# Performance work log

Hardware: AMD Instinct MI355X
Metric: run time of the kernel (lower is better)

Reference implementation:

```python
import jax, jax.numpy as jnp
from jax import lax
import numpy as np

NUM_ITER = 20
STOP_THRESH = 1e-4
NEG_SLOPE = 0.01


def _min_pool(x, window):
    # min over window == -max_pool(-x); stride 1, SAME padding matches pad=(k-1)//2
    return lax.reduce_window(x, jnp.inf, lax.min, (1, 1) + window, (1,) * 5, 'SAME')


def _max_pool(x, window):
    return lax.reduce_window(x, -jnp.inf, lax.max, (1, 1) + window, (1,) * 5, 'SAME')


def soft_erode(img):
    # kernels: (3,3,3) and (3,3,1) from anisotropy (1,1,0.5); both preserve shape
    e1 = _min_pool(img, (3, 3, 3))
    e2 = _min_pool(img, (3, 3, 1))
    return jnp.minimum(e1, e2)


def soft_dilate(img):
    return _max_pool(img, (3, 3, 3))


def soft_open(img):
    return soft_dilate(soft_erode(img))


def soft_skel(img):
    skel = jax.nn.leaky_relu(img - soft_open(img), NEG_SLOPE)
    prev = jnp.zeros_like(skel)
    active = jnp.asarray(True)

    def step(carry, _):
        cimg, cskel, cprev, cact = carry
        img2 = soft_erode(cimg)
        delta = jax.nn.leaky_relu(img2 - soft_open(img2), NEG_SLOPE)
        upd = jax.nn.leaky_relu(delta - cskel * delta, NEG_SLOPE)
        skel2 = cskel + upd
        dn = jnp.mean(jnp.abs(skel2 - cprev))
        # torch applies the update, THEN checks delta_norm and breaks; so the
        # update is applied whenever we were active entering the iteration.
        img_n = jnp.where(cact, img2, cimg)
        skel_n = jnp.where(cact, skel2, cskel)
        prev_n = jnp.where(cact, skel2, cprev)
        act_n = cact & (dn >= STOP_THRESH)
        return (img_n, skel_n, prev_n, act_n), None

    (_, skel, _, _), _ = lax.scan(step, (img, skel, prev, active), None, length=NUM_ITER)
    return skel


def setup_inputs() -> dict:
    key = jax.random.key(0)
    img = jax.random.uniform(key, (2, 1, 128, 256, 256), dtype=jnp.float32)
    return {"img": img}


def reference(img):
    # distance_transform returns zeros -> sigmoid(0)=0.5 path is absent since the
    # attribute is never set in __init__; forward is just soft_skel.
    return soft_skel(img)
```

## Files before the change

### kernel.cpp

```cpp
#include <hip/hip_runtime.h>
#include <math.h>

#define D_DIM 128
#define H_DIM 256
#define W_DIM 256
#define HW (H_DIM * W_DIM)
#define HW4 (HW / 4)
#define NIMG 2
#define NPI (D_DIM * HW)
#define NTOT (NIMG * NPI)

#define TDZ 32
#define TH 16
#define TW 64

#define AW4R 18
#define AW4 19
#define AH 20
#define EW4R 17
#define EW4 19
#define EH 18

#define NLOADLIN (AH * AW4)
#define NLOADP 384
#define NEPAIR ((EH / 2) * EW4R)

#define NUM_ITER 20
#define STOP_THRESH 1e-4

__device__ __forceinline__ float min3f(float a, float b, float c) { return fminf(fminf(a, b), c); }
__device__ __forceinline__ float max3f(float a, float b, float c) { return fmaxf(fmaxf(a, b), c); }
__device__ __forceinline__ float leaky(float x) { return fmaxf(x, 0.01f * x); }

__device__ __forceinline__ float dpp_shl1(float v) {
    int i = __float_as_int(v);
    int r = __builtin_amdgcn_update_dpp(i, i, 0x101, 0xF, 0xF, false);
    return __int_as_float(r);
}

#define BAR_FULL() do { asm volatile("s_waitcnt vmcnt(0) lgkmcnt(0)" ::: "memory"); \
                        __builtin_amdgcn_s_barrier(); \
                        __builtin_amdgcn_sched_barrier(0); } while (0)
#define BAR_VM4()  do { asm volatile("s_waitcnt vmcnt(4) lgkmcnt(0)" ::: "memory"); \
                        __builtin_amdgcn_s_barrier(); \
                        __builtin_amdgcn_sched_barrier(0); } while (0)
#define BAR_VM2()  do { asm volatile("s_waitcnt vmcnt(2) lgkmcnt(0)" ::: "memory"); \
                        __builtin_amdgcn_s_barrier(); \
                        __builtin_amdgcn_sched_barrier(0); } while (0)
#define BAR_LDS() do { asm volatile("s_waitcnt lgkmcnt(0)" ::: "memory"); \
                       __builtin_amdgcn_s_barrier(); \
                       __builtin_amdgcn_sched_barrier(0); } while (0)

#define GLOAD_LDS(gp, lp) \
    __builtin_amdgcn_global_load_lds((const __attribute__((address_space(1))) unsigned int*)(gp), \
                                     (__attribute__((address_space(3))) unsigned int*)(lp), 16, 0, 0)

__global__ void init_slots(double* slots) {
    int t = threadIdx.x;
    if (t < 32) slots[t] = 0.0;
    if (t >= 32 && t < 36) ((float*)(slots + 32))[t - 32] = INFINITY;
}

__global__ __launch_bounds__(256) void skel_step(
    const float* __restrict__ a_in,
    float* __restrict__ a_out,
    float* __restrict__ skel,
    double* __restrict__ slots,
    int step)
{
    __shared__ float4 aS4[4][NLOADP];
    __shared__ float4 eT4[2][EH * EW4];
    __shared__ float wsum[4];

    const int t = threadIdx.x;

    {
        int act = 1;
        for (int j = 1; j < step; ++j)
            if (!(slots[j] >= STOP_THRESH * (double)NTOT)) { act = 0; break; }
        if (!act) return;
    }

    const float* infp = (const float*)(slots + 32);

    const int lid = blockIdx.x + 4 * (blockIdx.y + 16 * blockIdx.z);
    const int swz = (lid & 7) * 64 + (lid >> 3);
    const int bx = swz & 3;
    const int by = (swz >> 2) & 15;
    const int zz = swz >> 6;
    const int bz = zz & 3, img = zz >> 2;
    const int x0 = bx * TW, y0 = by * TH, z0 = bz * TDZ;

    const float* in = a_in + (size_t)img * NPI;
    float4* aout4 = (float4*)(a_out + (size_t)img * NPI);
    float4* sk4 = (float4*)(skel + (size_t)img * NPI);

    int lOff0; bool lVal0;
    {
        int lr = t / AW4, lc = t - lr * AW4;
        int gy = y0 - 2 + lr, gx = x0 - 4 + 4 * lc;
        lVal0 = (lc < AW4R) && ((unsigned)gy < H_DIM) && ((unsigned)gx <= (unsigned)(W_DIM - 4));
        lOff0 = gy * W_DIM + gx;
    }
    const bool hasL1 = t < 128;
    int lOff1 = 0; bool lVal1 = false;
    if (hasL1) {
        int q = t + 256;
        int lr = q / AW4, lc = q - lr * AW4;
        int gy = y0 - 2 + lr, gx = x0 - 4 + 4 * lc;
        lVal1 = (q < NLOADLIN) && (lc < AW4R) && ((unsigned)gy < H_DIM)
                && ((unsigned)gx <= (unsigned)(W_DIM - 4));
        lOff1 = gy * W_DIM + gx;
    }
    const int wbase = (t >> 6) << 6;

    const bool isE = t < NEPAIR;
    int eRdP = 0, eWrP = 0;
    bool s0A = false, s0B = false, s0C = false, s0D = false;
    bool s1A = false, s1B = false, s1C = false, s1D = false;
    if (isE) {
        int rp = t / EW4R, ej = t - rp * EW4R;
        int mh0 = 2 * rp;
        eRdP = mh0 * AW4 + ej;
        eWrP = mh0 * EW4 + ej;
        int gy0e = y0 - 1 + mh0;
        bool g0 = (unsigned)gy0e < H_DIM;
        bool g1 = (unsigned)(gy0e + 1) < H_DIM;
        int gxb = x0 - 2 + 4 * ej;
        bool xA = (unsigned)(gxb + 0) < W_DIM;
        bool xB = (unsigned)(gxb + 1) < W_DIM;
        bool xC = (unsigned)(gxb + 2) < W_DIM;
        bool xD = (unsigned)(gxb + 3) < W_DIM;
        s0A = g0 && xA; s0B = g0 && xB; s0C = g0 && xC; s0D = g0 && xD;
        s1A = g1 && xA; s1B = g1 && xB; s1C = g1 && xC; s1D = g1 && xD;
    }

    const int oh = t >> 4, wq = t & 15;
    const bool isB = (wq == 15);
    const int oRd = oh * EW4 + wq;
    const int oAc = (oh + 2) * AW4 + wq + 1;
    size_t ob = ((size_t)z0 * HW + (size_t)(y0 + oh) * W_DIM + (size_t)x0) / 4 + wq;

    const float INF = INFINITY;
    const float4 ninf4 = make_float4(-INF, -INF, -INF, -INF);
    const float4 inf4 = make_float4(INF, INF, INF, INF);
    float4 m0P2 = inf4, m0P1 = inf4, m1P2 = inf4, m1P1 = inf4;
    float4 xP2 = ninf4, xP1 = ninf4;
    float4 acP2 = make_float4(0, 0, 0, 0), acP1 = acP2, ecP = acP2;
    float lsum = 0.f;

    for (int s = 0; s < 2; ++s) {
        int z = z0 - 2 + s;
        bool zok = (unsigned)z < D_DIM;
        const float* p = in + (size_t)z * HW;
        const float* s0 = (zok && lVal0) ? (p + lOff0) : infp;
        GLOAD_LDS(s0, &aS4[s][wbase]);
        if (hasL1) {
            const float* s1 = (zok && lVal1) ? (p + lOff1) : infp;
            GLOAD_LDS(s1, &aS4[s][256 + wbase]);
        }
    }

    #define ERODE_SLICE(SLOT, ZPV, DO_E, ETI, P2_0, P1_0, P2_1, P1_1)              \
    do { if (isE) {                                                                \
        const float4* s_ = aS4[SLOT];                                              \
        float4 a0 = s_[eRdP],           b0 = s_[eRdP + 1];                         \
        float4 a1 = s_[eRdP + AW4],     b1 = s_[eRdP + AW4 + 1];                   \
        float4 a2 = s_[eRdP + 2 * AW4], b2 = s_[eRdP + 2 * AW4 + 1];               \
        float4 a3 = s_[eRdP + 3 * AW4], b3 = s_[eRdP + 3 * AW4 + 1];               \
        float4 ma;                                                                 \
        ma.x = fminf(a1.x, a2.x); ma.y = fminf(a1.y, a2.y);                        \
        ma.z = fminf(a1.z, a2.z); ma.w = fminf(a1.w, a2.w);                        \
        float4 v0a, v1a;                                                           \
        v0a.x = fminf(a0.x, ma.x); v0a.y = fminf(a0.y, ma.y);                      \
        v0a.z = fminf(a0.z, ma.z); v0a.w = fminf(a0.w, ma.w);                      \
        v1a.x = fminf(a3.x, ma.x); v1a.y = fminf(a3.y, ma.y);                      \
        v1a.z = fminf(a3.z, ma.z); v1a.w = fminf(a3.w, ma.w);                      \
        float mbx = fminf(b1.x, b2.x), mby = fminf(b1.y, b2.y), mbz = fminf(b1.z, b2.z); \
        float v0bx = fminf(b0.x, mbx), v0by = fminf(b0.y, mby), v0bz = fminf(b0.z, mbz); \
        float v1bx = fminf(b3.x, mbx), v1by = fminf(b3.y, mby), v1bz = fminf(b3.z, mbz); \
        float4 mC0, mC1;                                                           \
        mC0.x = min3f(v0a.y, v0a.z, v0a.w);                                        \
        mC0.y = min3f(v0a.z, v0a.w, v0bx);                                         \
        mC0.z = min3f(v0a.w, v0bx, v0by);                                          \
        mC0.w = min3f(v0bx, v0by, v0bz);                                           \
        mC1.x = min3f(v1a.y, v1a.z, v1a.w);                                        \
        mC1.y = min3f(v1a.z, v1a.w, v1bx);                                         \
        mC1.z = min3f(v1a.w, v1bx, v1by);                                          \
        mC1.w = min3f(v1bx, v1by, v1bz);                                           \
        if ((DO_E) && (ZPV)) {                                                     \
            float4 e;                                                              \
            e.x = s0A ? min3f(P2_0.x, P1_0.x, mC0.x) : -INF;                       \
            e.y = s0B ? min3f(P2_0.y, P1_0.y, mC0.y) : -INF;                       \
            e.z = s0C ? min3f(P2_0.z, P1_0.z, mC0.z) : -INF;                       \
            e.w = s0D ? min3f(P2_0.w, P1_0.w, mC0.w) : -INF;                       \
            eT4[ETI][eWrP] = e;                                                    \
            e.x = s1A ? min3f(P2_1.x, P1_1.x, mC1.x) : -INF;                       \
            e.y = s1B ? min3f(P2_1.y, P1_1.y, mC1.y) : -INF;                       \
            e.z = s1C ? min3f(P2_1.z, P1_1.z, mC1.z) : -INF;                       \
            e.w = s1D ? min3f(P2_1.w, P1_1.w, mC1.w) : -INF;                       \
            eT4[ETI][eWrP + EW4] = e;                                              \
        }                                                                          \
        P2_0 = P1_0; P1_0 = mC0; P2_1 = P1_1; P1_1 = mC1;                          \
    } } while (0)

    #define MAX9(ETI, xCv, ecv)                                                    \
    do {                                                                           \
        const float4* eP_ = eT4[ETI];                                              \
        float4 A0 = eP_[oRd], A1 = eP_[oRd + EW4], A2 = eP_[oRd + 2 * EW4];        \
        float4 B0, B1, B2;                                                         \
        if (isB) {                                                                 \
            B0 = eP_[oRd + 1]; B1 = eP_[oRd + EW4 + 1]; B2 = eP_[oRd + 2 * EW4 + 1]; \
        }                                                                          \
        float4 vm;                                                                 \
        vm.x = max3f(A0.x, A1.x, A2.x); vm.y = max3f(A0.y, A1.y, A2.y);            \
        vm.z = max3f(A0.z, A1.z, A2.z); vm.w = max3f(A0.w, A1.w, A2.w);            \
        float sx = dpp_shl1(vm.x), sy = dpp_shl1(vm.y), sz = dpp_shl1(vm.z);       \
        float c1x = dpp_shl1(A1.x), c1y = dpp_shl1(A1.y);                          \
        float bvx = max3f(B0.x, B1.x, B2.x);                                       \
        float bvy = max3f(B0.y, B1.y, B2.y);                                       \
        float bvz = max3f(B0.z, B1.z, B2.z);                                       \
        float nbx = isB ? bvx : sx;                                                \
        float nby = isB ? bvy : sy;                                                \
        float nbz = isB ? bvz : sz;                                                \
        xCv.x = max3f(vm.y, vm.z, vm.w);                                           \
        xCv.y = max3f(vm.z, vm.w, nbx);                                            \
        xCv.z = max3f(vm.w, nbx, nby);                                             \
        xCv.w = max3f(nbx, nby, nbz);                                              \
        ecv.x = A1.z; ecv.y = A1.w;                                                \
        ecv.z = isB ? B1.x : c1x;                                                  \
        ecv.w = isB ? B1.y : c1y;                                                  \
    } while (0)

    for (int k = 0; k < (TDZ + 4) / 2; ++k) {
        const int i0 = 2 * k, i1 = 2 * k + 1;
        const int slot0 = i0 & 3, slot1 = i1 & 3;

        if (k < 3) { BAR_FULL(); }
        else if (step == NUM_ITER) { BAR_VM2(); }
        else { BAR_VM4(); }

        float4 ggPre0, ggPre1;
        if (step > 0 && i0 >= 4) { ggPre0 = sk4[ob]; ggPre1 = sk4[ob + HW4]; }
        __builtin_amdgcn_sched_barrier(0);

        if (k <= (TDZ + 4) / 2 - 2) {
            for (int s = 0; s < 2; ++s) {
                int z = z0 + 2 * k + s;
                bool zok = (unsigned)z < D_DIM;
                const float* p = in + (size_t)z * HW;
                const float* s0 = (zok && lVal0) ? (p + lOff0) : infp;
                GLOAD_LDS(s0, &aS4[(i0 + 2 + s) & 3][wbase]);
                if (hasL1) {
                    const float* s1 = (zok && lVal1) ? (p + lOff1) : infp;
                    GLOAD_LDS(s1, &aS4[(i0 + 2 + s) & 3][256 + wbase]);
                }
            }
        }
        __builtin_amdgcn_sched_barrier(0);

        const bool zp0 = (unsigned)(z0 - 3 + i0) < D_DIM;
        const bool zp1 = (unsigned)(z0 - 3 + i1) < D_DIM;
        const bool doE = (i0 >= 2);

        ERODE_SLICE(slot0, zp0, doE, 0, m0P2, m0P1, m1P2, m1P1);
        ERODE_SLICE(slot1, zp1, (i1 >= 2), 1, m0P2, m0P1, m1P2, m1P1);

        const float4 aCn0 = aS4[slot0][oAc];
        const float4 aCn1 = aS4[slot1][oAc];

        BAR_LDS();

        {
            float4 xC0, ecB0, xC1, ecB1;
            if (doE && zp0) { MAX9(0, xC0, ecB0); } else { xC0 = ninf4; ecB0 = ninf4; }
            if (doE && zp1) { MAX9(1, xC1, ecB1); } else { xC1 = ninf4; ecB1 = ninf4; }

            if (i0 >= 4) {
                {
                    float4 dl;
                    dl.x = leaky(acP2.x - max3f(xP2.x, xP1.x, xC0.x));
                    dl.y = leaky(acP2.y - max3f(xP2.y, xP1.y, xC0.y));
                    dl.z = leaky(acP2.z - max3f(xP2.z, xP1.z, xC0.z));
                    dl.w = leaky(acP2.w - max3f(xP2.w, xP1.w, xC0.w));
                    if (step < NUM_ITER) aout4[ob] = ecP;
                    if (step == 0) {
                        sk4[ob] = dl;
                    } else {
                        float4 gg = ggPre0, up, gn;
                        up.x = leaky(dl.x - gg.x * dl.x); gn.x = gg.x + up.x;
                        up.y = leaky(dl.y - gg.y * dl.y); gn.y = gg.y + up.y;
                        up.z = leaky(dl.z - gg.z * dl.z); gn.z = gg.z + up.z;
                        up.w = leaky(dl.w - gg.w * dl.w); gn.w = gg.w + up.w;
                        sk4[ob] = gn;
                        if (step == 1)
                            lsum += fabsf(gn.x) + fabsf(gn.y) + fabsf(gn.z) + fabsf(gn.w);
                        else
                            lsum += fabsf(up.x) + fabsf(up.y) + fabsf(up.z) + fabsf(up.w);
                    }
                }
                {
                    float4 dl;
                    dl.x = leaky(acP1.x - max3f(xP1.x, xC0.x, xC1.x));
                    dl.y = leaky(acP1.y - max3f(xP1.y, xC0.y, xC1.y));
                    dl.z = leaky(acP1.z - max3f(xP1.z, xC0.z, xC1.z));
                    dl.w = leaky(acP1.w - max3f(xP1.w, xC0.w, xC1.w));
                    if (step < NUM_ITER) aout4[ob + HW4] = ecB0;
                    if (step == 0) {
                        sk4[ob + HW4] = dl;
                    } else {
                        float4 gg = ggPre1, up, gn;
                        up.x = leaky(dl.x - gg.x * dl.x); gn.x = gg.x + up.x;
                        up.y = leaky(dl.y - gg.y * dl.y); gn.y = gg.y + up.y;
                        up.z = leaky(dl.z - gg.z * dl.z); gn.z = gg.z + up.z;
                        up.w = leaky(dl.w - gg.w * dl.w); gn.w = gg.w + up.w;
                        sk4[ob + HW4] = gn;
                        if (step == 1)
                            lsum += fabsf(gn.x) + fabsf(gn.y) + fabsf(gn.z) + fabsf(gn.w);
                        else
                            lsum += fabsf(up.x) + fabsf(up.y) + fabsf(up.z) + fabsf(up.w);
                    }
                }
                ob += 2 * HW4;
            }
            xP2 = xC0; xP1 = xC1;
            acP2 = aCn0; acP1 = aCn1;
            ecP = ecB1;
        }
    }

    #undef ERODE_SLICE
    #undef MAX9

    if (step > 0) {
        #pragma unroll
        for (int off = 32; off > 0; off >>= 1)
            lsum += __shfl_down(lsum, off, 64);
        const int lane = t & 63, wid = t >> 6;
        if (lane == 0) wsum[wid] = lsum;
        __syncthreads();
        if (t == 0) {
            float b = wsum[0] + wsum[1] + wsum[2] + wsum[3];
            atomicAdd(&slots[step], (double)b);
        }
    }
}

extern "C" void kernel_launch(void* const* d_in, const int* in_sizes, int n_in,
                              void* d_out, int out_size, void* d_ws, size_t ws_size,
                              hipStream_t stream) {
    const float* img = (const float*)d_in[0];
    float* out = (float*)d_out;
    float* buf0 = (float*)d_ws;
    float* buf1 = buf0 + NTOT;
    double* slots = (double*)(buf1 + NTOT);

    init_slots<<<1, 64, 0, stream>>>(slots);

    dim3 grid(W_DIM / TW, H_DIM / TH, (D_DIM / TDZ) * NIMG);
    for (int s = 0; s <= NUM_ITER; ++s) {
        const float* ain = (s == 0) ? img : ((s & 1) ? buf0 : buf1);
        float* aout = (s & 1) ? buf1 : buf0;
        skel_step<<<grid, 256, 0, stream>>>(ain, aout, out, slots, s);
    }
}
```

Measured before the change: 324.8 us.

## Compute two output rows per thread in half-wave layout to share vertical max

The output phase now assigns two adjacent output rows to each active thread, and only the lower 32 lanes of each wave take part. The vertical 3-row max shares the middle two rows between both outputs, cutting LDS reads and max operations per output. The global wait counts grow to match the doubled stores and loads in flight. The trade-off is that half of each wave sits idle in the output stage, and register pressure rises.

```diff
diff --git a/kernel.cpp b/kernel.cpp
--- a/kernel.cpp
+++ b/kernel.cpp
@@ -32,6 +32,13 @@
 __device__ __forceinline__ float max3f(float a, float b, float c) { return fmaxf(fmaxf(a, b), c); }
 __device__ __forceinline__ float leaky(float x) { return fmaxf(x, 0.01f * x); }
 
+__device__ __forceinline__ float4 f4max3v(float4 a, float4 b, float4 c) {
+    float4 r;
+    r.x = max3f(a.x, b.x, c.x); r.y = max3f(a.y, b.y, c.y);
+    r.z = max3f(a.z, b.z, c.z); r.w = max3f(a.w, b.w, c.w);
+    return r;
+}
+
 __device__ __forceinline__ float dpp_shl1(float v) {
     int i = __float_as_int(v);
     int r = __builtin_amdgcn_update_dpp(i, i, 0x101, 0xF, 0xF, false);
@@ -41,10 +48,7 @@
 #define BAR_FULL() do { asm volatile("s_waitcnt vmcnt(0) lgkmcnt(0)" ::: "memory"); \
                         __builtin_amdgcn_s_barrier(); \
                         __builtin_amdgcn_sched_barrier(0); } while (0)
-#define BAR_VM4()  do { asm volatile("s_waitcnt vmcnt(4) lgkmcnt(0)" ::: "memory"); \
-                        __builtin_amdgcn_s_barrier(); \
-                        __builtin_amdgcn_sched_barrier(0); } while (0)
-#define BAR_VM2()  do { asm volatile("s_waitcnt vmcnt(2) lgkmcnt(0)" ::: "memory"); \
+#define BAR_VMN(N) do { asm volatile("s_waitcnt vmcnt(" #N ") lgkmcnt(0)" ::: "memory"); \
                         __builtin_amdgcn_s_barrier(); \
                         __builtin_amdgcn_sched_barrier(0); } while (0)
 #define BAR_LDS() do { asm volatile("s_waitcnt lgkmcnt(0)" ::: "memory"); \
@@ -135,18 +139,26 @@
         s1A = g1 && xA; s1B = g1 && xB; s1C = g1 && xC; s1D = g1 && xD;
     }
 
-    const int oh = t >> 4, wq = t & 15;
+    const int wv = t >> 6, ln = t & 63;
+    const bool isO = ln < 32;
+    const int oq = (wv << 5) | (ln & 31);
+    const int orp = oq >> 4;
+    const int wq = oq & 15;
     const bool isB = (wq == 15);
-    const int oRd = oh * EW4 + wq;
-    const int oAc = (oh + 2) * AW4 + wq + 1;
-    size_t ob = ((size_t)z0 * HW + (size_t)(y0 + oh) * W_DIM + (size_t)x0) / 4 + wq;
+    const int oRdP = (2 * orp) * EW4 + wq;
+    const int oAc0 = (2 * orp + 2) * AW4 + wq + 1;
+    const int oAc1 = oAc0 + AW4;
+    size_t ob0 = ((size_t)z0 * HW + (size_t)(y0 + 2 * orp) * W_DIM + x0) / 4 + wq;
+    size_t ob1 = ob0 + (W_DIM / 4);
 
     const float INF = INFINITY;
     const float4 ninf4 = make_float4(-INF, -INF, -INF, -INF);
     const float4 inf4 = make_float4(INF, INF, INF, INF);
     float4 m0P2 = inf4, m0P1 = inf4, m1P2 = inf4, m1P1 = inf4;
-    float4 xP2 = ninf4, xP1 = ninf4;
-    float4 acP2 = make_float4(0, 0, 0, 0), acP1 = acP2, ecP = acP2;
+    float4 x0P2 = ninf4, x0P1 = ninf4, x1P2 = ninf4, x1P1 = ninf4;
+    float4 ac0P2 = make_float4(0, 0, 0, 0), ac0P1 = ac0P2;
+    float4 ac1P2 = ac0P2, ac1P1 = ac0P2;
+    float4 ecP0 = ac0P2, ecP1 = ac0P2;
     float lsum = 0.f;
 
     for (int s = 0; s < 2; ++s) {
@@ -204,32 +216,71 @@
         P2_0 = P1_0; P1_0 = mC0; P2_1 = P1_1; P1_1 = mC1;                          \
     } } while (0)
 
-    #define MAX9(ETI, xCv, ecv)                                                    \
+    #define MAX9P(ETI, xC0v, xC1v, ec0v, ec1v)                                     \
     do {                                                                           \
         const float4* eP_ = eT4[ETI];                                              \
-        float4 A0 = eP_[oRd], A1 = eP_[oRd + EW4], A2 = eP_[oRd + 2 * EW4];        \
-        float4 B0, B1, B2;                                                         \
+        float4 A0 = eP_[oRdP],           A1 = eP_[oRdP + EW4];                     \
+        float4 A2 = eP_[oRdP + 2 * EW4], A3 = eP_[oRdP + 3 * EW4];                 \
+        float4 B0 = ninf4, B1 = ninf4, B2 = ninf4, B3 = ninf4;                     \
         if (isB) {                                                                 \
-            B0 = eP_[oRd + 1]; B1 = eP_[oRd + EW4 + 1]; B2 = eP_[oRd + 2 * EW4 + 1]; \
+            B0 = eP_[oRdP + 1];           B1 = eP_[oRdP + EW4 + 1];                \
+            B2 = eP_[oRdP + 2 * EW4 + 1]; B3 = eP_[oRdP + 3 * EW4 + 1];            \
         }                                                                          \
-        float4 vm;                                                                 \
-        vm.x = max3f(A0.x, A1.x, A2.x); vm.y = max3f(A0.y, A1.y, A2.y);            \
-        vm.z = max3f(A0.z, A1.z, A2.z); vm.w = max3f(A0.w, A1.w, A2.w);            \
-        float sx = dpp_shl1(vm.x), sy = dpp_shl1(vm.y), sz = dpp_shl1(vm.z);       \
+        float4 mm;                                                                 \
+        mm.x = fmaxf(A1.x, A2.x); mm.y = fmaxf(A1.y, A2.y);                        \
+        mm.z = fmaxf(A1.z, A2.z); mm.w = fmaxf(A1.w, A2.w);                        \
+        float4 vm0, vm1;                                                           \
+        vm0.x = fmaxf(A0.x, mm.x); vm0.y = fmaxf(A0.y, mm.y);                      \
+        vm0.z = fmaxf(A0.z, mm.z); vm0.w = fmaxf(A0.w, mm.w);                      \
+        vm1.x = fmaxf(A3.x, mm.x); vm1.y = fmaxf(A3.y, mm.y);                      \
+        vm1.z = fmaxf(A3.z, mm.z); vm1.w = fmaxf(A3.w, mm.w);                      \
+        float s0x = dpp_shl1(vm0.x), s0y = dpp_shl1(vm0.y), s0z = dpp_shl1(vm0.z); \
+        float s1x = dpp_shl1(vm1.x), s1y = dpp_shl1(vm1.y), s1z = dpp_shl1(vm1.z); \
         float c1x = dpp_shl1(A1.x), c1y = dpp_shl1(A1.y);                          \
-        float bvx = max3f(B0.x, B1.x, B2.x);                                       \
-        float bvy = max3f(B0.y, B1.y, B2.y);                                       \
-        float bvz = max3f(B0.z, B1.z, B2.z);                                       \
-        float nbx = isB ? bvx : sx;                                                \
-        float nby = isB ? bvy : sy;                                                \
-        float nbz = isB ? bvz : sz;                                                \
-        xCv.x = max3f(vm.y, vm.z, vm.w);                                           \
-        xCv.y = max3f(vm.z, vm.w, nbx);                                            \
-        xCv.z = max3f(vm.w, nbx, nby);                                             \
-        xCv.w = max3f(nbx, nby, nbz);                                              \
-        ecv.x = A1.z; ecv.y = A1.w;                                                \
-        ecv.z = isB ? B1.x : c1x;                                                  \
-        ecv.w = isB ? B1.y : c1y;                                                  \
+        float c2x = dpp_shl1(A2.x), c2y = dpp_shl1(A2.y);                          \
+        float bv0x = max3f(B0.x, B1.x, B2.x);                                      \
+        float bv0y = max3f(B0.y, B1.y, B2.y);                                      \
+        float bv0z = max3f(B0.z, B1.z, B2.z);                                      \
+        float bv1x = max3f(B1.x, B2.x, B3.x);                                      \
+        float bv1y = max3f(B1.y, B2.y, B3.y);                                      \
+        float bv1z = max3f(B1.z, B2.z, B3.z);                                      \
+        float n0x = isB ? bv0x : s0x, n0y = isB ? bv0y : s0y, n0z = isB ? bv0z : s0z; \
+        float n1x = isB ? bv1x : s1x, n1y = isB ? bv1y : s1y, n1z = isB ? bv1z : s1z; \
+        xC0v.x = max3f(vm0.y, vm0.z, vm0.w);                                       \
+        xC0v.y = max3f(vm0.z, vm0.w, n0x);                                         \
+        xC0v.z = max3f(vm0.w, n0x, n0y);                                           \
+        xC0v.w = max3f(n0x, n0y, n0z);                                             \
+        xC1v.x = max3f(vm1.y, vm1.z, vm1.w);                                       \
+        xC1v.y = max3f(vm1.z, vm1.w, n1x);                                         \
+        xC1v.z = max3f(vm1.w, n1x, n1y);                                           \
+        xC1v.w = max3f(n1x, n1y, n1z);                                             \
+        ec0v.x = A1.z; ec0v.y = A1.w;                                              \
+        ec0v.z = isB ? B1.x : c1x; ec0v.w = isB ? B1.y : c1y;                      \
+        ec1v.x = A2.z; ec1v.y = A2.w;                                              \
+        ec1v.z = isB ? B2.x : c2x; ec1v.w = isB ? B2.y : c2y;                      \
+    } while (0)
+
+    #define OUT1(OB, GG, ACv, XA, XB, XC, ECW)                                     \
+    do {                                                                           \
+        float4 dm = f4max3v(XA, XB, XC);                                           \
+        float4 dl;                                                                 \
+        dl.x = leaky(ACv.x - dm.x); dl.y = leaky(ACv.y - dm.y);                    \
+        dl.z = leaky(ACv.z - dm.z); dl.w = leaky(ACv.w - dm.w);                    \
+        if (step < NUM_ITER) aout4[OB] = ECW;                                      \
+        if (step == 0) {                                                           \
+            sk4[OB] = dl;                                                          \
+        } else {                                                                   \
+            float4 gg = GG, up, gn;                                                \
+            up.x = leaky(dl.x - gg.x * dl.x); gn.x = gg.x + up.x;                  \
+            up.y = leaky(dl.y - gg.y * dl.y); gn.y = gg.y + up.y;                  \
+            up.z = leaky(dl.z - gg.z * dl.z); gn.z = gg.z + up.z;                  \
+            up.w = leaky(dl.w - gg.w * dl.w); gn.w = gg.w + up.w;                  \
+            sk4[OB] = gn;                                                          \
+            if (step == 1)                                                         \
+                lsum += fabsf(gn.x) + fabsf(gn.y) + fabsf(gn.z) + fabsf(gn.w);     \
+            else                                                                   \
+                lsum += fabsf(up.x) + fabsf(up.y) + fabsf(up.z) + fabsf(up.w);     \
+        }                                                                          \
     } while (0)
 
     for (int k = 0; k < (TDZ + 4) / 2; ++k) {
@@ -237,11 +288,14 @@
         const int slot0 = i0 & 3, slot1 = i1 & 3;
 
         if (k < 3) { BAR_FULL(); }
-        else if (step == NUM_ITER) { BAR_VM2(); }
-        else { BAR_VM4(); }
-
-        float4 ggPre0, ggPre1;
-        if (step > 0 && i0 >= 4) { ggPre0 = sk4[ob]; ggPre1 = sk4[ob + HW4]; }
+        else if (step == NUM_ITER) { BAR_VMN(4); }
+        else { BAR_VMN(8); }
+
+        float4 ggP00, ggP01, ggP10, ggP11;
+        if (step > 0 && i0 >= 4 && isO) {
+            ggP00 = sk4[ob0]; ggP01 = sk4[ob0 + HW4];
+            ggP10 = sk4[ob1]; ggP11 = sk4[ob1 + HW4];
+        }
         __builtin_amdgcn_sched_barrier(0);
 
         if (k <= (TDZ + 4) / 2 - 2) {
@@ -266,71 +320,37 @@
         ERODE_SLICE(slot0, zp0, doE, 0, m0P2, m0P1, m1P2, m1P1);
         ERODE_SLICE(slot1, zp1, (i1 >= 2), 1, m0P2, m0P1, m1P2, m1P1);
 
-        const float4 aCn0 = aS4[slot0][oAc];
-        const float4 aCn1 = aS4[slot1][oAc];
+        float4 aA0, aA1, aB0, aB1;
+        if (isO) {
+            aA0 = aS4[slot0][oAc0]; aA1 = aS4[slot0][oAc1];
+            aB0 = aS4[slot1][oAc0]; aB1 = aS4[slot1][oAc1];
+        }
 
         BAR_LDS();
 
-        {
-            float4 xC0, ecB0, xC1, ecB1;
-            if (doE && zp0) { MAX9(0, xC0, ecB0); } else { xC0 = ninf4; ecB0 = ninf4; }
-            if (doE && zp1) { MAX9(1, xC1, ecB1); } else { xC1 = ninf4; ecB1 = ninf4; }
+        if (isO) {
+            float4 xCA0, xCA1, ecA0, ecA1, xCB0, xCB1, ecB0, ecB1;
+            if (doE && zp0) { MAX9P(0, xCA0, xCA1, ecA0, ecA1); }
+            else { xCA0 = ninf4; xCA1 = ninf4; ecA0 = ninf4; ecA1 = ninf4; }
+            if (doE && zp1) { MAX9P(1, xCB0, xCB1, ecB0, ecB1); }
+            else { xCB0 = ninf4; xCB1 = ninf4; ecB0 = ninf4; ecB1 = ninf4; }
 
             if (i0 >= 4) {
-                {
-                    float4 dl;
-                    dl.x = leaky(acP2.x - max3f(xP2.x, xP1.x, xC0.x));
-                    dl.y = leaky(acP2.y - max3f(xP2.y, xP1.y, xC0.y));
-                    dl.z = leaky(acP2.z - max3f(xP2.z, xP1.z, xC0.z));
-                    dl.w = leaky(acP2.w - max3f(xP2.w, xP1.w, xC0.w));
-                    if (step < NUM_ITER) aout4[ob] = ecP;
-                    if (step == 0) {
-                        sk4[ob] = dl;
-                    } else {
-                        float4 gg = ggPre0, up, gn;
-                        up.x = leaky(dl.x - gg.x * dl.x); gn.x = gg.x + up.x;
-                        up.y = leaky(dl.y - gg.y * dl.y); gn.y = gg.y + up.y;
-                        up.z = leaky(dl.z - gg.z * dl.z); gn.z = gg.z + up.z;
-                        up.w = leaky(dl.w - gg.w * dl.w); gn.w = gg.w + up.w;
-                        sk4[ob] = gn;
-                        if (step == 1)
-                            lsum += fabsf(gn.x) + fabsf(gn.y) + fabsf(gn.z) + fabsf(gn.w);
-                        else
-                            lsum += fabsf(up.x) + fabsf(up.y) + fabsf(up.z) + fabsf(up.w);
-                    }
-                }
-                {
-                    float4 dl;
-                    dl.x = leaky(acP1.x - max3f(xP1.x, xC0.x, xC1.x));
-                    dl.y = leaky(acP1.y - max3f(xP1.y, xC0.y, xC1.y));
-                    dl.z = leaky(acP1.z - max3f(xP1.z, xC0.z, xC1.z));
-                    dl.w = leaky(acP1.w - max3f(xP1.w, xC0.w, xC1.w));
-                    if (step < NUM_ITER) aout4[ob + HW4] = ecB0;
-                    if (step == 0) {
-                        sk4[ob + HW4] = dl;
-                    } else {
-                        float4 gg = ggPre1, up, gn;
-                        up.x = leaky(dl.x - gg.x * dl.x); gn.x = gg.x + up.x;
-                        up.y = leaky(dl.y - gg.y * dl.y); gn.y = gg.y + up.y;
-                        up.z = leaky(dl.z - gg.z * dl.z); gn.z = gg.z + up.z;
-                        up.w = leaky(dl.w - gg.w * dl.w); gn.w = gg.w + up.w;
-                        sk4[ob + HW4] = gn;
-                        if (step == 1)
-                            lsum += fabsf(gn.x) + fabsf(gn.y) + fabsf(gn.z) + fabsf(gn.w);
-                        else
-                            lsum += fabsf(up.x) + fabsf(up.y) + fabsf(up.z) + fabsf(up.w);
-                    }
-                }
-                ob += 2 * HW4;
+                OUT1(ob0,       ggP00, ac0P2, x0P2, x0P1, xCA0, ecP0);
+                OUT1(ob0 + HW4, ggP01, ac0P1, x0P1, xCA0, xCB0, ecA0);
+                OUT1(ob1,       ggP10, ac1P2, x1P2, x1P1, xCA1, ecP1);
+                OUT1(ob1 + HW4, ggP11, ac1P1, x1P1, xCA1, xCB1, ecA1);
+                ob0 += 2 * HW4; ob1 += 2 * HW4;
             }
-            xP2 = xC0; xP1 = xC1;
-            acP2 = aCn0; acP1 = aCn1;
-            ecP = ecB1;
+            x0P2 = xCA0; x0P1 = xCB0; x1P2 = xCA1; x1P1 = xCB1;
+            ac0P2 = aA0; ac0P1 = aB0; ac1P2 = aA1; ac1P1 = aB1;
+            ecP0 = ecB0; ecP1 = ecB1;
         }
     }
 
     #undef ERODE_SLICE
-    #undef MAX9
+    #undef MAX9P
+    #undef OUT1
 
     if (step > 0) {
         #pragma unroll
```

Result: slower. 421.9 us (+29.9%).
